# Optimization experiments

Measured on AMD Instinct MI355X. Metric: run time of the kernel, lower is better.

The kernel has to match this reference:

```python
import jax, jax.numpy as jnp
import numpy as np

H, N, I, K = 1024, 16, 128, 2  # model dim, n_experts, expert inner dim (hardcoded in Expert), top-k
B, S = 4, 4096


def setup_inputs() -> dict:
    key = jax.random.key(0)
    ks = jax.random.split(key, 4)
    x = jax.random.normal(ks[0], (B, S, H), jnp.float32)
    Wr = jax.random.normal(ks[1], (N, H), jnp.float32) / np.sqrt(H)      # router Linear(h,n,bias=False) weight [n,h]
    Wg = jax.random.normal(ks[2], (N, I, H), jnp.float32) / np.sqrt(H)   # per-expert g: Linear(h,i) weight [i,h]
    bg = jnp.zeros((N, I), jnp.float32)
    Wu = jax.random.normal(ks[3], (N, H, I), jnp.float32) / np.sqrt(I)   # per-expert u: Linear(i,h) weight [h,i]
    bu = jnp.zeros((N, H), jnp.float32)
    return {"x": x, "Wr": Wr, "Wg": Wg, "bg": bg, "Wu": Wu, "bu": bu, "k": K}


def reference(x, Wr, Wg, bg, Wu, bu, k):
    b, s, h = x.shape
    n = Wr.shape[0]
    xf = x.reshape(-1, h)                      # [T, h]
    T = xf.shape[0]
    logits = xf @ Wr.T                          # [T, n]
    val, idx = jax.lax.top_k(logits, k)         # [T, k]
    w = jax.nn.softmax(val, axis=-1)            # softmax over selected top-k logits
    # scatter top-k weights into a dense [T, n] gate matrix (zero for unselected experts)
    gates = jnp.zeros((T, n), x.dtype).at[jnp.arange(T)[:, None], idx].set(w)
    # all-expert SwiGLU-free MLP: silu(x @ Wg^T + bg) @ Wu^T + bu, weighted combine by gates
    a = jax.nn.silu(jnp.einsum('th,nih->tni', xf, Wg) + bg)   # [T, n, i]
    out = jnp.einsum('tn,tni,nhi->th', gates, a, Wu) + gates @ bu
    return out.reshape(b, s, h)
```

## Files before the change

### kernel.cpp

```cpp
#include <hip/hip_runtime.h>
#include <hip/hip_fp16.h>

#define T_TOK 16384
#define HDIM  1024
#define NE    16
#define IDIM  128
#define BMq   64
#define NSLOT (T_TOK*2)
#define NSLOT_PAD (NSLOT + NE*BMq)
#define NBLK1 (NSLOT_PAD/BMq)

typedef _Float16 half8 __attribute__((ext_vector_type(8)));
typedef _Float16 half4 __attribute__((ext_vector_type(4)));
typedef float    f32x4 __attribute__((ext_vector_type(4)));

#define WS_TOKE 0
#define WS_TOKW 131072
#define WS_CNT  262144
#define WS_CUR  262208
#define WS_OFF  262272
#define WS_STOK 262400
#define WS_SW   397568
#define WS_ABUF 532736
#define WS_TSLOT 9183488ULL
#define WS_WG16  9314560ULL
#define WS_WU16  13508864ULL
#define WS_X16   17703168ULL
#define WS_OBUF  51257600ULL
#define WS_FULL_END 120463616ULL

template<bool WX>
__global__ __launch_bounds__(256) void router_k(const float* __restrict__ x,
                                                const float* __restrict__ Wr,
                                                int2* __restrict__ tok_e,
                                                float2* __restrict__ tok_w,
                                                _Float16* __restrict__ x16) {
    int wv = threadIdx.x >> 6, lane = threadIdx.x & 63;
#pragma unroll
    for (int i = 0; i < 2; ++i) {
        int t = blockIdx.x * 4 + wv + i * 8192;
        float acc[NE];
#pragma unroll
        for (int e = 0; e < NE; ++e) acc[e] = 0.f;
        const float4* xp = reinterpret_cast<const float4*>(x + (size_t)t * HDIM);
#pragma unroll
        for (int p = 0; p < 4; ++p) {
            int off = p * 64 + lane;
            float4 xv = xp[off];
            if (WX) {
                half4 hv = {(_Float16)xv.x,(_Float16)xv.y,(_Float16)xv.z,(_Float16)xv.w};
                *reinterpret_cast<half4*>(x16 + (size_t)t * HDIM + off * 4) = hv;
            }
#pragma unroll
            for (int e = 0; e < NE; ++e) {
                float4 wv4 = *reinterpret_cast<const float4*>(Wr + (size_t)e * HDIM + off * 4);
                acc[e] += xv.x*wv4.x + xv.y*wv4.y + xv.z*wv4.z + xv.w*wv4.w;
            }
        }
#pragma unroll
        for (int e = 0; e < NE; ++e) {
#pragma unroll
            for (int m = 1; m < 64; m <<= 1)
                acc[e] += __shfl_xor(acc[e], m);
        }
        if (lane == 0) {
            float v1 = -1e30f, v2 = -1e30f; int i1 = 0, i2 = 0;
#pragma unroll
            for (int q = 0; q < NE; ++q) {
                float lv = acc[q];
                if (lv > v1)      { v2 = v1; i2 = i1; v1 = lv; i1 = q; }
                else if (lv > v2) { v2 = lv; i2 = q; }
            }
            float e2 = __expf(v2 - v1);
            float inv = 1.f / (1.f + e2);
            tok_e[t] = make_int2(i1, i2);
            tok_w[t] = make_float2(inv, e2 * inv);
        }
    }
}

__global__ __launch_bounds__(256) void cvtw_k(const float* __restrict__ Wg,
                                              const float* __restrict__ Wu,
                                              _Float16* __restrict__ Wg16,
                                              _Float16* __restrict__ Wu16) {
    int i = blockIdx.x * 256 + threadIdx.x;
    float4 g = reinterpret_cast<const float4*>(Wg)[i];
    float4 u = reinterpret_cast<const float4*>(Wu)[i];
    half4 gh = {(_Float16)g.x,(_Float16)g.y,(_Float16)g.z,(_Float16)g.w};
    half4 uh = {(_Float16)u.x,(_Float16)u.y,(_Float16)u.z,(_Float16)u.w};
    reinterpret_cast<half4*>(Wg16)[i] = gh;
    reinterpret_cast<half4*>(Wu16)[i] = uh;
}

__global__ __launch_bounds__(256) void count_k(const int2* __restrict__ tok_e,
                                               int* __restrict__ counts) {
    int e = blockIdx.x;
    int c = 0;
    for (int t = threadIdx.x; t < T_TOK; t += 256) {
        int2 te = tok_e[t];
        c += (te.x == e) + (te.y == e);
    }
    __shared__ int red[256];
    red[threadIdx.x] = c; __syncthreads();
    for (int s = 128; s > 0; s >>= 1) {
        if (threadIdx.x < s) red[threadIdx.x] += red[threadIdx.x + s];
        __syncthreads();
    }
    if (threadIdx.x == 0) counts[e] = red[0];
}

__global__ void scan_k(const int* __restrict__ counts, int* __restrict__ offs) {
    if (threadIdx.x == 0) {
        int acc = 0;
        for (int e = 0; e < NE; ++e) {
            offs[e] = acc;
            acc += ((counts[e] + BMq - 1) / BMq) * BMq;
        }
        offs[NE] = acc;
    }
}

template<bool FULL>
__global__ __launch_bounds__(256) void scatter_k(const int2* __restrict__ tok_e,
                                                 const float2* __restrict__ tok_w,
                                                 const int* __restrict__ offs,
                                                 int* __restrict__ cursors,
                                                 int* __restrict__ slot_tok,
                                                 float* __restrict__ slot_w,
                                                 int2* __restrict__ tok_slots) {
    __shared__ int lcnt[NE];
    __shared__ int lbase[NE];
    if (threadIdx.x < NE) lcnt[threadIdx.x] = 0;
    __syncthreads();
    int t = blockIdx.x * 256 + threadIdx.x;
    int2 te = tok_e[t]; float2 tw = tok_w[t];
    int p0 = atomicAdd(&lcnt[te.x], 1);
    int p1 = atomicAdd(&lcnt[te.y], 1);
    __syncthreads();
    if (threadIdx.x < NE)
        lbase[threadIdx.x] = atomicAdd(&cursors[threadIdx.x], lcnt[threadIdx.x]);
    __syncthreads();
    int s0 = offs[te.x] + lbase[te.x] + p0;
    int s1 = offs[te.y] + lbase[te.y] + p1;
    slot_tok[s0] = t; slot_w[s0] = tw.x;
    slot_tok[s1] = t; slot_w[s1] = tw.y;
    if (FULL) tok_slots[t] = make_int2(s0, s1);
}

template<bool FULL>
__global__ __launch_bounds__(256) void gemm1_k(const float* __restrict__ x,
                                               const _Float16* __restrict__ x16,
                                               const float* __restrict__ Wg,
                                               const _Float16* __restrict__ Wg16,
                                               const float* __restrict__ bg,
                                               const int* __restrict__ offs,
                                               const int* __restrict__ slot_tok,
                                               _Float16* __restrict__ abuf) {
    __shared__ __align__(16) _Float16 As[64 * 64];
    __shared__ __align__(16) _Float16 Bs[128 * 64];
    __shared__ int tokLds[64];
    int row0 = blockIdx.x * BMq;
    if (row0 >= offs[NE]) return;
    int e = 0;
#pragma unroll
    for (int q = 1; q < NE; ++q) if (offs[q] <= row0) e = q;
    int tid = threadIdx.x;
    if (tid < 64) tokLds[tid] = slot_tok[row0 + tid];
    __syncthreads();
    int wv = tid >> 6, lane = tid & 63;
    f32x4 acc[4][2] = {};
    for (int kk = 0; kk < HDIM; kk += 64) {
        if (FULL) {
#pragma unroll
            for (int j = 0; j < 2; ++j) {
                int idx = tid + j * 256;
                int r = idx >> 3, hq = idx & 7;
                int tok = tokLds[r];
                half8 v = {0,0,0,0,0,0,0,0};
                if (tok >= 0) v = *reinterpret_cast<const half8*>(x16 + (size_t)tok * HDIM + kk + hq * 8);
                *reinterpret_cast<half8*>(&As[r * 64 + ((hq * 8) ^ ((r & 7) << 3))]) = v;
            }
#pragma unroll
            for (int j = 0; j < 4; ++j) {
                int idx = tid + j * 256;
                int r = idx >> 3, hq = idx & 7;
                half8 v = *reinterpret_cast<const half8*>(Wg16 + (size_t)e * IDIM * HDIM + (size_t)r * HDIM + kk + hq * 8);
                *reinterpret_cast<half8*>(&Bs[r * 64 + ((hq * 8) ^ ((r & 7) << 3))]) = v;
            }
        } else {
#pragma unroll
            for (int j = 0; j < 4; ++j) {
                int idx = tid + j * 256;
                int r = idx >> 4, kq = idx & 15;
                int tok = tokLds[r];
                float4 v = make_float4(0.f, 0.f, 0.f, 0.f);
                if (tok >= 0) v = *reinterpret_cast<const float4*>(x + (size_t)tok * HDIM + kk + kq * 4);
                half4 hv = {(_Float16)v.x, (_Float16)v.y, (_Float16)v.z, (_Float16)v.w};
                *reinterpret_cast<half4*>(&As[r * 64 + ((kq * 4) ^ ((r & 7) << 3))]) = hv;
            }
#pragma unroll 4
            for (int j = 0; j < 8; ++j) {
                int idx = tid + j * 256;
                int r = idx >> 4, kq = idx & 15;
                float4 v = *reinterpret_cast<const float4*>(Wg + (size_t)e * IDIM * HDIM + (size_t)r * HDIM + kk + kq * 4);
                half4 hv = {(_Float16)v.x, (_Float16)v.y, (_Float16)v.z, (_Float16)v.w};
                *reinterpret_cast<half4*>(&Bs[r * 64 + ((kq * 4) ^ ((r & 7) << 3))]) = hv;
            }
        }
        __syncthreads();
#pragma unroll
        for (int ks = 0; ks < 64; ks += 32) {
            int c = ks + ((lane >> 4) << 3);
            half8 af[4], bf[2];
#pragma unroll
            for (int rt = 0; rt < 4; ++rt) {
                int r = rt * 16 + (lane & 15);
                af[rt] = *reinterpret_cast<const half8*>(&As[r * 64 + (c ^ ((r & 7) << 3))]);
            }
#pragma unroll
            for (int ct = 0; ct < 2; ++ct) {
                int r = wv * 32 + ct * 16 + (lane & 15);
                bf[ct] = *reinterpret_cast<const half8*>(&Bs[r * 64 + (c ^ ((r & 7) << 3))]);
            }
#pragma unroll
            for (int rt = 0; rt < 4; ++rt)
#pragma unroll
                for (int ct = 0; ct < 2; ++ct)
                    acc[rt][ct] = __builtin_amdgcn_mfma_f32_16x16x32_f16(af[rt], bf[ct], acc[rt][ct], 0, 0, 0);
        }
        __syncthreads();
    }
#pragma unroll
    for (int rt = 0; rt < 4; ++rt)
#pragma unroll
        for (int ct = 0; ct < 2; ++ct) {
            int i = wv * 32 + ct * 16 + (lane & 15);
            float bgv = bg[e * IDIM + i];
#pragma unroll
            for (int j = 0; j < 4; ++j) {
                int m = rt * 16 + ((lane >> 4) << 2) + j;
                if (tokLds[m] >= 0) {
                    float v = acc[rt][ct][j] + bgv;
                    float sv = v / (1.f + __expf(-v));
                    abuf[(size_t)(row0 + m) * IDIM + i] = (_Float16)sv;
                }
            }
        }
}

template<bool FULL>
__global__ __launch_bounds__(256) void gemm2_k(const _Float16* __restrict__ abuf,
                                               const float* __restrict__ Wu,
                                               const _Float16* __restrict__ Wu16,
                                               const float* __restrict__ bu,
                                               const int* __restrict__ offs,
                                               const int* __restrict__ slot_tok,
                                               const float* __restrict__ slot_w,
                                               float* __restrict__ out,
                                               _Float16* __restrict__ Obuf) {
    __shared__ __align__(16) _Float16 As[64 * 128];
    __shared__ __align__(16) _Float16 Bs[128 * 128];
    __shared__ int   tokLds[64];
    __shared__ float wLds[64];
    int row0 = blockIdx.x * BMq;
    if (row0 >= offs[NE]) return;
    int h0 = blockIdx.y * 128;
    int e = 0;
#pragma unroll
    for (int q = 1; q < NE; ++q) if (offs[q] <= row0) e = q;
    int tid = threadIdx.x;
    if (tid < 64) { tokLds[tid] = slot_tok[row0 + tid]; wLds[tid] = slot_w[row0 + tid]; }
#pragma unroll
    for (int j = 0; j < 4; ++j) {
        int idx = tid + j * 256;
        int r = idx >> 4, hq = idx & 15;
        half8 v = *reinterpret_cast<const half8*>(abuf + (size_t)(row0 + r) * IDIM + hq * 8);
        *reinterpret_cast<half8*>(&As[r * 128 + ((hq * 8) ^ ((r & 7) << 3))]) = v;
    }
    if (FULL) {
#pragma unroll
        for (int j = 0; j < 8; ++j) {
            int idx = tid + j * 256;
            int r = idx >> 4, fq = idx & 15;
            half8 v = *reinterpret_cast<const half8*>(Wu16 + (size_t)e * HDIM * IDIM + (size_t)(h0 + r) * IDIM + fq * 8);
            *reinterpret_cast<half8*>(&Bs[r * 128 + ((fq * 8) ^ ((r & 7) << 3))]) = v;
        }
    } else {
#pragma unroll 4
        for (int j = 0; j < 16; ++j) {
            int idx = tid + j * 256;
            int r = idx >> 5, fq = idx & 31;
            float4 v = *reinterpret_cast<const float4*>(Wu + (size_t)e * HDIM * IDIM + (size_t)(h0 + r) * IDIM + fq * 4);
            half4 hv = {(_Float16)v.x, (_Float16)v.y, (_Float16)v.z, (_Float16)v.w};
            *reinterpret_cast<half4*>(&Bs[r * 128 + ((fq * 4) ^ ((r & 7) << 3))]) = hv;
        }
    }
    __syncthreads();
    int wv = tid >> 6, lane = tid & 63;
    f32x4 acc[4][2] = {};
#pragma unroll
    for (int ks = 0; ks < 128; ks += 32) {
        int c = ks + ((lane >> 4) << 3);
        half8 af[4], bf[2];
#pragma unroll
        for (int rt = 0; rt < 4; ++rt) {
            int r = rt * 16 + (lane & 15);
            af[rt] = *reinterpret_cast<const half8*>(&As[r * 128 + (c ^ ((r & 7) << 3))]);
        }
#pragma unroll
        for (int ct = 0; ct < 2; ++ct) {
            int r = wv * 32 + ct * 16 + (lane & 15);
            bf[ct] = *reinterpret_cast<const half8*>(&Bs[r * 128 + (c ^ ((r & 7) << 3))]);
        }
#pragma unroll
        for (int rt = 0; rt < 4; ++rt)
#pragma unroll
            for (int ct = 0; ct < 2; ++ct)
                acc[rt][ct] = __builtin_amdgcn_mfma_f32_16x16x32_f16(af[rt], bf[ct], acc[rt][ct], 0, 0, 0);
    }
#pragma unroll
    for (int rt = 0; rt < 4; ++rt)
#pragma unroll
        for (int ct = 0; ct < 2; ++ct) {
            int h = h0 + wv * 32 + ct * 16 + (lane & 15);
#pragma unroll
            for (int j = 0; j < 4; ++j) {
                int m = rt * 16 + ((lane >> 4) << 2) + j;
                if (FULL) {
                    Obuf[(size_t)(row0 + m) * HDIM + h] = (_Float16)acc[rt][ct][j];
                } else {
                    int tok = tokLds[m];
                    if (tok >= 0)
                        atomicAdd(out + (size_t)tok * HDIM + h,
                                  (acc[rt][ct][j] + bu[e * HDIM + h]) * wLds[m]);
                }
            }
        }
}

__global__ __launch_bounds__(256) void combine_k(const _Float16* __restrict__ Obuf,
                                                 const float* __restrict__ bu,
                                                 const int2* __restrict__ tok_slots,
                                                 const int2* __restrict__ tok_e,
                                                 const float2* __restrict__ tok_w,
                                                 float* __restrict__ out) {
    int wv = threadIdx.x >> 6, lane = threadIdx.x & 63;
    int t = blockIdx.x * 4 + wv;
    int2   sl = tok_slots[t];
    int2   te = tok_e[t];
    float2 tw = tok_w[t];
    const _Float16* O1 = Obuf + (size_t)sl.x * HDIM;
    const _Float16* O2 = Obuf + (size_t)sl.y * HDIM;
    const float* b1 = bu + (size_t)te.x * HDIM;
    const float* b2 = bu + (size_t)te.y * HDIM;
    float* op = out + (size_t)t * HDIM;
#pragma unroll
    for (int q = 0; q < 4; ++q) {
        int h = q * 256 + lane * 4;
        half4  a1 = *reinterpret_cast<const half4*>(O1 + h);
        half4  a2 = *reinterpret_cast<const half4*>(O2 + h);
        float4 v1 = *reinterpret_cast<const float4*>(b1 + h);
        float4 v2 = *reinterpret_cast<const float4*>(b2 + h);
        float4 o;
        o.x = tw.x * ((float)a1[0] + v1.x) + tw.y * ((float)a2[0] + v2.x);
        o.y = tw.x * ((float)a1[1] + v1.y) + tw.y * ((float)a2[1] + v2.y);
        o.z = tw.x * ((float)a1[2] + v1.z) + tw.y * ((float)a2[2] + v2.z);
        o.w = tw.x * ((float)a1[3] + v1.w) + tw.y * ((float)a2[3] + v2.w);
        *reinterpret_cast<float4*>(op + h) = o;
    }
}

extern "C" void kernel_launch(void* const* d_in, const int* in_sizes, int n_in,
                              void* d_out, int out_size, void* d_ws, size_t ws_size,
                              hipStream_t stream) {
    const float* x  = (const float*)d_in[0];
    const float* Wr = (const float*)d_in[1];
    const float* Wg = (const float*)d_in[2];
    const float* bg = (const float*)d_in[3];
    const float* Wu = (const float*)d_in[4];
    const float* bu = (const float*)d_in[5];
    float* out = (float*)d_out;
    char* ws = (char*)d_ws;

    int2*      tok_e    = (int2*)(ws + WS_TOKE);
    float2*    tok_w    = (float2*)(ws + WS_TOKW);
    int*       counts   = (int*)(ws + WS_CNT);
    int*       cursors  = (int*)(ws + WS_CUR);
    int*       offs     = (int*)(ws + WS_OFF);
    int*       slot_tok = (int*)(ws + WS_STOK);
    float*     slot_w   = (float*)(ws + WS_SW);
    _Float16*  abuf     = (_Float16*)(ws + WS_ABUF);
    int2*      tok_slots= (int2*)(ws + WS_TSLOT);
    _Float16*  Wg16     = (_Float16*)(ws + WS_WG16);
    _Float16*  Wu16     = (_Float16*)(ws + WS_WU16);
    _Float16*  x16      = (_Float16*)(ws + WS_X16);
    _Float16*  Obuf     = (_Float16*)(ws + WS_OBUF);

    const bool full = (ws_size >= WS_FULL_END);

    hipMemsetAsync(ws + WS_CNT, 0, 256, stream);
    hipMemsetAsync(slot_tok, 0xFF, NSLOT_PAD * sizeof(int), stream);

    if (full) {
        cvtw_k   <<<2048, 256, 0, stream>>>(Wg, Wu, Wg16, Wu16);
        router_k<true><<<T_TOK/8, 256, 0, stream>>>(x, Wr, tok_e, tok_w, x16);
        count_k  <<<NE, 256, 0, stream>>>(tok_e, counts);
        scan_k   <<<1, 64, 0, stream>>>(counts, offs);
        scatter_k<true><<<T_TOK/256, 256, 0, stream>>>(tok_e, tok_w, offs, cursors, slot_tok, slot_w, tok_slots);
        gemm1_k<true><<<NBLK1, 256, 0, stream>>>(x, x16, Wg, Wg16, bg, offs, slot_tok, abuf);
        dim3 g2(NBLK1, 8);
        gemm2_k<true><<<g2, 256, 0, stream>>>(abuf, Wu, Wu16, bu, offs, slot_tok, slot_w, out, Obuf);
        combine_k<<<T_TOK/4, 256, 0, stream>>>(Obuf, bu, tok_slots, tok_e, tok_w, out);
    } else {
        hipMemsetAsync(d_out, 0, (size_t)T_TOK * HDIM * sizeof(float), stream);
        router_k<false><<<T_TOK/8, 256, 0, stream>>>(x, Wr, tok_e, tok_w, nullptr);
        count_k  <<<NE, 256, 0, stream>>>(tok_e, counts);
        scan_k   <<<1, 64, 0, stream>>>(counts, offs);
        scatter_k<false><<<T_TOK/256, 256, 0, stream>>>(tok_e, tok_w, offs, cursors, slot_tok, slot_w, nullptr);
        gemm1_k<false><<<NBLK1, 256, 0, stream>>>(x, nullptr, Wg, nullptr, bg, offs, slot_tok, abuf);
        dim3 g2(NBLK1, 8);
        gemm2_k<false><<<g2, 256, 0, stream>>>(abuf, Wu, nullptr, bu, offs, slot_tok, slot_w, out, nullptr);
    }
}
```

Measured before the change: 274.8 us.

## Fuse routing count and slot init into MFMA router; drop weight pre-conversion

The router is rewritten to compute logits with fp16 MFMA instructions, using a hi/lo split of x and Wr to keep near-fp32 accuracy. It also builds a per-block expert histogram, which replaces the separate count kernel, and initialises slot_tok, which replaces a memset. The separate fp16 weight-conversion kernel is removed, so the GEMMs convert fp32 weights on the fly. The bu bias add moves from combine into gemm2's epilogue. This cuts launches and a full extra pass over the weights, at the cost of more conversion work and heavier fp32 weight loads inside the GEMMs.

```diff
diff --git a/kernel.cpp b/kernel.cpp
--- a/kernel.cpp
+++ b/kernel.cpp
@@ -23,90 +23,82 @@
 #define WS_SW   397568
 #define WS_ABUF 532736
 #define WS_TSLOT 9183488ULL
-#define WS_WG16  9314560ULL
-#define WS_WU16  13508864ULL
 #define WS_X16   17703168ULL
 #define WS_OBUF  51257600ULL
 #define WS_FULL_END 120463616ULL
+
+__device__ inline void hilo8(float4 a, float4 b, half8& h, half8& l) {
+    float f[8] = {a.x, a.y, a.z, a.w, b.x, b.y, b.z, b.w};
+#pragma unroll
+    for (int i = 0; i < 8; ++i) {
+        _Float16 hi = (_Float16)f[i];
+        h[i] = hi;
+        l[i] = (_Float16)((f[i] - (float)hi) * 2048.f);
+    }
+}
 
 template<bool WX>
 __global__ __launch_bounds__(256) void router_k(const float* __restrict__ x,
                                                 const float* __restrict__ Wr,
                                                 int2* __restrict__ tok_e,
                                                 float2* __restrict__ tok_w,
-                                                _Float16* __restrict__ x16) {
-    int wv = threadIdx.x >> 6, lane = threadIdx.x & 63;
-#pragma unroll
-    for (int i = 0; i < 2; ++i) {
-        int t = blockIdx.x * 4 + wv + i * 8192;
-        float acc[NE];
-#pragma unroll
-        for (int e = 0; e < NE; ++e) acc[e] = 0.f;
-        const float4* xp = reinterpret_cast<const float4*>(x + (size_t)t * HDIM);
-#pragma unroll
-        for (int p = 0; p < 4; ++p) {
-            int off = p * 64 + lane;
-            float4 xv = xp[off];
-            if (WX) {
-                half4 hv = {(_Float16)xv.x,(_Float16)xv.y,(_Float16)xv.z,(_Float16)xv.w};
-                *reinterpret_cast<half4*>(x16 + (size_t)t * HDIM + off * 4) = hv;
-            }
-#pragma unroll
-            for (int e = 0; e < NE; ++e) {
-                float4 wv4 = *reinterpret_cast<const float4*>(Wr + (size_t)e * HDIM + off * 4);
-                acc[e] += xv.x*wv4.x + xv.y*wv4.y + xv.z*wv4.z + xv.w*wv4.w;
-            }
-        }
-#pragma unroll
-        for (int e = 0; e < NE; ++e) {
-#pragma unroll
-            for (int m = 1; m < 64; m <<= 1)
-                acc[e] += __shfl_xor(acc[e], m);
-        }
-        if (lane == 0) {
-            float v1 = -1e30f, v2 = -1e30f; int i1 = 0, i2 = 0;
-#pragma unroll
-            for (int q = 0; q < NE; ++q) {
-                float lv = acc[q];
-                if (lv > v1)      { v2 = v1; i2 = i1; v1 = lv; i1 = q; }
-                else if (lv > v2) { v2 = lv; i2 = q; }
-            }
-            float e2 = __expf(v2 - v1);
-            float inv = 1.f / (1.f + e2);
-            tok_e[t] = make_int2(i1, i2);
-            tok_w[t] = make_float2(inv, e2 * inv);
-        }
-    }
-}
-
-__global__ __launch_bounds__(256) void cvtw_k(const float* __restrict__ Wg,
-                                              const float* __restrict__ Wu,
-                                              _Float16* __restrict__ Wg16,
-                                              _Float16* __restrict__ Wu16) {
-    int i = blockIdx.x * 256 + threadIdx.x;
-    float4 g = reinterpret_cast<const float4*>(Wg)[i];
-    float4 u = reinterpret_cast<const float4*>(Wu)[i];
-    half4 gh = {(_Float16)g.x,(_Float16)g.y,(_Float16)g.z,(_Float16)g.w};
-    half4 uh = {(_Float16)u.x,(_Float16)u.y,(_Float16)u.z,(_Float16)u.w};
-    reinterpret_cast<half4*>(Wg16)[i] = gh;
-    reinterpret_cast<half4*>(Wu16)[i] = uh;
-}
-
-__global__ __launch_bounds__(256) void count_k(const int2* __restrict__ tok_e,
-                                               int* __restrict__ counts) {
-    int e = blockIdx.x;
-    int c = 0;
-    for (int t = threadIdx.x; t < T_TOK; t += 256) {
-        int2 te = tok_e[t];
-        c += (te.x == e) + (te.y == e);
-    }
-    __shared__ int red[256];
-    red[threadIdx.x] = c; __syncthreads();
-    for (int s = 128; s > 0; s >>= 1) {
-        if (threadIdx.x < s) red[threadIdx.x] += red[threadIdx.x + s];
-        __syncthreads();
-    }
-    if (threadIdx.x == 0) counts[e] = red[0];
+                                                _Float16* __restrict__ x16,
+                                                int* __restrict__ counts,
+                                                int* __restrict__ slot_tok) {
+    __shared__ float red[4][16][16];
+    __shared__ int hist[NE];
+    int tid = threadIdx.x;
+    int wv = tid >> 6, lane = tid & 63;
+    int tile0 = blockIdx.x * 16;
+
+    int gi = blockIdx.x * 256 + tid;
+    if (gi < NSLOT_PAD) slot_tok[gi] = -1;
+    if (tid < NE) hist[tid] = 0;
+
+    int row = lane & 15;
+    int kq  = (lane >> 4) * 8;
+    const float* xrow = x  + (size_t)(tile0 + row) * HDIM;
+    const float* wrow = Wr + (size_t)row * HDIM;
+    f32x4 accM = {0.f,0.f,0.f,0.f};
+    f32x4 accC = {0.f,0.f,0.f,0.f};
+#pragma unroll
+    for (int s = 0; s < 8; ++s) {
+        int k = wv * 256 + s * 32 + kq;
+        float4 xa = *reinterpret_cast<const float4*>(xrow + k);
+        float4 xb = *reinterpret_cast<const float4*>(xrow + k + 4);
+        float4 wa = *reinterpret_cast<const float4*>(wrow + k);
+        float4 wb = *reinterpret_cast<const float4*>(wrow + k + 4);
+        half8 xh, xl, wh, wl;
+        hilo8(xa, xb, xh, xl);
+        hilo8(wa, wb, wh, wl);
+        if (WX)
+            *reinterpret_cast<half8*>(x16 + (size_t)(tile0 + row) * HDIM + k) = xh;
+        accM = __builtin_amdgcn_mfma_f32_16x16x32_f16(xh, wh, accM, 0, 0, 0);
+        accC = __builtin_amdgcn_mfma_f32_16x16x32_f16(xh, wl, accC, 0, 0, 0);
+        accC = __builtin_amdgcn_mfma_f32_16x16x32_f16(xl, wh, accC, 0, 0, 0);
+    }
+#pragma unroll
+    for (int j = 0; j < 4; ++j)
+        red[wv][(lane >> 4) * 4 + j][lane & 15] = accM[j] + accC[j] * (1.f/2048.f);
+    __syncthreads();
+    if (tid < 16) {
+        float v1 = -1e30f, v2 = -1e30f; int i1 = 0, i2 = 0;
+#pragma unroll
+        for (int q = 0; q < NE; ++q) {
+            float lv = red[0][tid][q] + red[1][tid][q] + red[2][tid][q] + red[3][tid][q];
+            if (lv > v1)      { v2 = v1; i2 = i1; v1 = lv; i1 = q; }
+            else if (lv > v2) { v2 = lv; i2 = q; }
+        }
+        int t = tile0 + tid;
+        float e2 = __expf(v2 - v1);
+        float inv = 1.f / (1.f + e2);
+        tok_e[t] = make_int2(i1, i2);
+        tok_w[t] = make_float2(inv, e2 * inv);
+        atomicAdd(&hist[i1], 1);
+        atomicAdd(&hist[i2], 1);
+    }
+    __syncthreads();
+    if (tid < NE) { int c = hist[tid]; if (c) atomicAdd(&counts[tid], c); }
 }
 
 __global__ void scan_k(const int* __restrict__ counts, int* __restrict__ offs) {
@@ -151,7 +143,6 @@
 __global__ __launch_bounds__(256) void gemm1_k(const float* __restrict__ x,
                                                const _Float16* __restrict__ x16,
                                                const float* __restrict__ Wg,
-                                               const _Float16* __restrict__ Wg16,
                                                const float* __restrict__ bg,
                                                const int* __restrict__ offs,
                                                const int* __restrict__ slot_tok,
@@ -180,13 +171,6 @@
                 if (tok >= 0) v = *reinterpret_cast<const half8*>(x16 + (size_t)tok * HDIM + kk + hq * 8);
                 *reinterpret_cast<half8*>(&As[r * 64 + ((hq * 8) ^ ((r & 7) << 3))]) = v;
             }
-#pragma unroll
-            for (int j = 0; j < 4; ++j) {
-                int idx = tid + j * 256;
-                int r = idx >> 3, hq = idx & 7;
-                half8 v = *reinterpret_cast<const half8*>(Wg16 + (size_t)e * IDIM * HDIM + (size_t)r * HDIM + kk + hq * 8);
-                *reinterpret_cast<half8*>(&Bs[r * 64 + ((hq * 8) ^ ((r & 7) << 3))]) = v;
-            }
         } else {
 #pragma unroll
             for (int j = 0; j < 4; ++j) {
@@ -198,14 +182,14 @@
                 half4 hv = {(_Float16)v.x, (_Float16)v.y, (_Float16)v.z, (_Float16)v.w};
                 *reinterpret_cast<half4*>(&As[r * 64 + ((kq * 4) ^ ((r & 7) << 3))]) = hv;
             }
+        }
 #pragma unroll 4
-            for (int j = 0; j < 8; ++j) {
-                int idx = tid + j * 256;
-                int r = idx >> 4, kq = idx & 15;
-                float4 v = *reinterpret_cast<const float4*>(Wg + (size_t)e * IDIM * HDIM + (size_t)r * HDIM + kk + kq * 4);
-                half4 hv = {(_Float16)v.x, (_Float16)v.y, (_Float16)v.z, (_Float16)v.w};
-                *reinterpret_cast<half4*>(&Bs[r * 64 + ((kq * 4) ^ ((r & 7) << 3))]) = hv;
-            }
+        for (int j = 0; j < 8; ++j) {
+            int idx = tid + j * 256;
+            int r = idx >> 4, kq = idx & 15;
+            float4 v = *reinterpret_cast<const float4*>(Wg + (size_t)e * IDIM * HDIM + (size_t)r * HDIM + kk + kq * 4);
+            half4 hv = {(_Float16)v.x, (_Float16)v.y, (_Float16)v.z, (_Float16)v.w};
+            *reinterpret_cast<half4*>(&Bs[r * 64 + ((kq * 4) ^ ((r & 7) << 3))]) = hv;
         }
         __syncthreads();
 #pragma unroll
@@ -251,7 +235,6 @@
 template<bool FULL>
 __global__ __launch_bounds__(256) void gemm2_k(const _Float16* __restrict__ abuf,
                                                const float* __restrict__ Wu,
-                                               const _Float16* __restrict__ Wu16,
                                                const float* __restrict__ bu,
                                                const int* __restrict__ offs,
                                                const int* __restrict__ slot_tok,
@@ -277,23 +260,13 @@
         half8 v = *reinterpret_cast<const half8*>(abuf + (size_t)(row0 + r) * IDIM + hq * 8);
         *reinterpret_cast<half8*>(&As[r * 128 + ((hq * 8) ^ ((r & 7) << 3))]) = v;
     }
-    if (FULL) {
-#pragma unroll
-        for (int j = 0; j < 8; ++j) {
-            int idx = tid + j * 256;
-            int r = idx >> 4, fq = idx & 15;
-            half8 v = *reinterpret_cast<const half8*>(Wu16 + (size_t)e * HDIM * IDIM + (size_t)(h0 + r) * IDIM + fq * 8);
-            *reinterpret_cast<half8*>(&Bs[r * 128 + ((fq * 8) ^ ((r & 7) << 3))]) = v;
-        }
-    } else {
 #pragma unroll 4
-        for (int j = 0; j < 16; ++j) {
-            int idx = tid + j * 256;
-            int r = idx >> 5, fq = idx & 31;
-            float4 v = *reinterpret_cast<const float4*>(Wu + (size_t)e * HDIM * IDIM + (size_t)(h0 + r) * IDIM + fq * 4);
-            half4 hv = {(_Float16)v.x, (_Float16)v.y, (_Float16)v.z, (_Float16)v.w};
-            *reinterpret_cast<half4*>(&Bs[r * 128 + ((fq * 4) ^ ((r & 7) << 3))]) = hv;
-        }
+    for (int j = 0; j < 16; ++j) {
+        int idx = tid + j * 256;
+        int r = idx >> 5, fq = idx & 31;
+        float4 v = *reinterpret_cast<const float4*>(Wu + (size_t)e * HDIM * IDIM + (size_t)(h0 + r) * IDIM + fq * 4);
+        half4 hv = {(_Float16)v.x, (_Float16)v.y, (_Float16)v.z, (_Float16)v.w};
+        *reinterpret_cast<half4*>(&Bs[r * 128 + ((fq * 4) ^ ((r & 7) << 3))]) = hv;
     }
     __syncthreads();
     int wv = tid >> 6, lane = tid & 63;
@@ -323,49 +296,43 @@
 #pragma unroll
         for (int ct = 0; ct < 2; ++ct) {
             int h = h0 + wv * 32 + ct * 16 + (lane & 15);
+            float buv = bu[e * HDIM + h];
 #pragma unroll
             for (int j = 0; j < 4; ++j) {
                 int m = rt * 16 + ((lane >> 4) << 2) + j;
                 if (FULL) {
-                    Obuf[(size_t)(row0 + m) * HDIM + h] = (_Float16)acc[rt][ct][j];
+                    Obuf[(size_t)(row0 + m) * HDIM + h] = (_Float16)(acc[rt][ct][j] + buv);
                 } else {
                     int tok = tokLds[m];
                     if (tok >= 0)
                         atomicAdd(out + (size_t)tok * HDIM + h,
-                                  (acc[rt][ct][j] + bu[e * HDIM + h]) * wLds[m]);
+                                  (acc[rt][ct][j] + buv) * wLds[m]);
                 }
             }
         }
 }
 
 __global__ __launch_bounds__(256) void combine_k(const _Float16* __restrict__ Obuf,
-                                                 const float* __restrict__ bu,
                                                  const int2* __restrict__ tok_slots,
-                                                 const int2* __restrict__ tok_e,
                                                  const float2* __restrict__ tok_w,
                                                  float* __restrict__ out) {
     int wv = threadIdx.x >> 6, lane = threadIdx.x & 63;
     int t = blockIdx.x * 4 + wv;
     int2   sl = tok_slots[t];
-    int2   te = tok_e[t];
     float2 tw = tok_w[t];
     const _Float16* O1 = Obuf + (size_t)sl.x * HDIM;
     const _Float16* O2 = Obuf + (size_t)sl.y * HDIM;
-    const float* b1 = bu + (size_t)te.x * HDIM;
-    const float* b2 = bu + (size_t)te.y * HDIM;
     float* op = out + (size_t)t * HDIM;
 #pragma unroll
     for (int q = 0; q < 4; ++q) {
         int h = q * 256 + lane * 4;
         half4  a1 = *reinterpret_cast<const half4*>(O1 + h);
         half4  a2 = *reinterpret_cast<const half4*>(O2 + h);
-        float4 v1 = *reinterpret_cast<const float4*>(b1 + h);
-        float4 v2 = *reinterpret_cast<const float4*>(b2 + h);
         float4 o;
-        o.x = tw.x * ((float)a1[0] + v1.x) + tw.y * ((float)a2[0] + v2.x);
-        o.y = tw.x * ((float)a1[1] + v1.y) + tw.y * ((float)a2[1] + v2.y);
-        o.z = tw.x * ((float)a1[2] + v1.z) + tw.y * ((float)a2[2] + v2.z);
-        o.w = tw.x * ((float)a1[3] + v1.w) + tw.y * ((float)a2[3] + v2.w);
+        o.x = tw.x * (float)a1[0] + tw.y * (float)a2[0];
+        o.y = tw.x * (float)a1[1] + tw.y * (float)a2[1];
+        o.z = tw.x * (float)a1[2] + tw.y * (float)a2[2];
+        o.w = tw.x * (float)a1[3] + tw.y * (float)a2[3];
         *reinterpret_cast<float4*>(op + h) = o;
     }
 }
@@ -391,34 +358,28 @@
     float*     slot_w   = (float*)(ws + WS_SW);
     _Float16*  abuf     = (_Float16*)(ws + WS_ABUF);
     int2*      tok_slots= (int2*)(ws + WS_TSLOT);
-    _Float16*  Wg16     = (_Float16*)(ws + WS_WG16);
-    _Float16*  Wu16     = (_Float16*)(ws + WS_WU16);
     _Float16*  x16      = (_Float16*)(ws + WS_X16);
     _Float16*  Obuf     = (_Float16*)(ws + WS_OBUF);
 
     const bool full = (ws_size >= WS_FULL_END);
 
     hipMemsetAsync(ws + WS_CNT, 0, 256, stream);
-    hipMemsetAsync(slot_tok, 0xFF, NSLOT_PAD * sizeof(int), stream);
 
     if (full) {
-        cvtw_k   <<<2048, 256, 0, stream>>>(Wg, Wu, Wg16, Wu16);
-        router_k<true><<<T_TOK/8, 256, 0, stream>>>(x, Wr, tok_e, tok_w, x16);
-        count_k  <<<NE, 256, 0, stream>>>(tok_e, counts);
+        router_k<true><<<T_TOK/16, 256, 0, stream>>>(x, Wr, tok_e, tok_w, x16, counts, slot_tok);
         scan_k   <<<1, 64, 0, stream>>>(counts, offs);
         scatter_k<true><<<T_TOK/256, 256, 0, stream>>>(tok_e, tok_w, offs, cursors, slot_tok, slot_w, tok_slots);
-        gemm1_k<true><<<NBLK1, 256, 0, stream>>>(x, x16, Wg, Wg16, bg, offs, slot_tok, abuf);
+        gemm1_k<true><<<NBLK1, 256, 0, stream>>>(x, x16, Wg, bg, offs, slot_tok, abuf);
         dim3 g2(NBLK1, 8);
-        gemm2_k<true><<<g2, 256, 0, stream>>>(abuf, Wu, Wu16, bu, offs, slot_tok, slot_w, out, Obuf);
-        combine_k<<<T_TOK/4, 256, 0, stream>>>(Obuf, bu, tok_slots, tok_e, tok_w, out);
+        gemm2_k<true><<<g2, 256, 0, stream>>>(abuf, Wu, bu, offs, slot_tok, slot_w, out, Obuf);
+        combine_k<<<T_TOK/4, 256, 0, stream>>>(Obuf, tok_slots, tok_w, out);
     } else {
         hipMemsetAsync(d_out, 0, (size_t)T_TOK * HDIM * sizeof(float), stream);
-        router_k<false><<<T_TOK/8, 256, 0, stream>>>(x, Wr, tok_e, tok_w, nullptr);
-        count_k  <<<NE, 256, 0, stream>>>(tok_e, counts);
+        router_k<false><<<T_TOK/16, 256, 0, stream>>>(x, Wr, tok_e, tok_w, nullptr, counts, slot_tok);
         scan_k   <<<1, 64, 0, stream>>>(counts, offs);
         scatter_k<false><<<T_TOK/256, 256, 0, stream>>>(tok_e, tok_w, offs, cursors, slot_tok, slot_w, nullptr);
-        gemm1_k<false><<<NBLK1, 256, 0, stream>>>(x, nullptr, Wg, nullptr, bg, offs, slot_tok, abuf);
+        gemm1_k<false><<<NBLK1, 256, 0, stream>>>(x, nullptr, Wg, bg, offs, slot_tok, abuf);
         dim3 g2(NBLK1, 8);
-        gemm2_k<false><<<g2, 256, 0, stream>>>(abuf, Wu, nullptr, bu, offs, slot_tok, slot_w, out, nullptr);
-    }
-}
+        gemm2_k<false><<<g2, 256, 0, stream>>>(abuf, Wu, bu, offs, slot_tok, slot_w, out, nullptr);
+    }
+}
```

New measurement: 274.4 us. No clear change (-0.1%).
